# Kernel tuning notes

Hardware: AMD Instinct MI355X
Metric: run time of the kernel (lower is better)

## Reference

```python
import jax, jax.numpy as jnp
import numpy as np

SAMPLE_RATE = 24000.0
HARMONIC_NUM = 8
SINE_AMP = 0.1


def setup_inputs() -> dict:
    key = jax.random.key(0)
    k_f0, k_uv, k_w, k_b, k_n = jax.random.split(key, 5)
    batch, frames, upp = 16, 1000, 300
    f0_hz = 100.0 + 300.0 * jax.random.uniform(k_f0, (batch, frames), dtype=jnp.float32)
    voiced = jax.random.uniform(k_uv, (batch, frames)) > 0.2
    f0 = jnp.where(voiced, f0_hz, 0.0).astype(jnp.float32)
    W = jax.random.normal(k_w, (1, HARMONIC_NUM + 1), dtype=jnp.float32) / 3.0
    b = jax.random.normal(k_b, (1,), dtype=jnp.float32) * 0.01
    noise = jax.random.normal(k_n, (batch, frames * upp, 1), dtype=jnp.float32)
    return {"f0": f0, "W": W, "b": b, "noise": noise, "upp": upp}


def reference(f0, W, b, noise, upp):
    # Nearest-neighbor upsample along time: [B, F] -> [B, F*upp]
    f0_up = jnp.repeat(f0, upp, axis=1)
    # cumsum(f0 * h) == h * cumsum(f0): one scan, broadcast over harmonics.
    base_phase = jnp.cumsum(f0_up / SAMPLE_RATE, axis=1) * (2.0 * np.pi)  # [B, S]
    h = jnp.arange(1, HARMONIC_NUM + 2, dtype=f0.dtype)  # [9]
    sines = jnp.sin(base_phase[..., None] * h) * SINE_AMP  # [B, S, 9]
    uv = (f0_up > 0).astype(f0.dtype)[..., None]  # [B, S, 1]
    harmonics = sines * uv
    har_source = jnp.tanh(jnp.einsum('bsh,oh->bso', harmonics, W) + b)  # [B, S, 1]
    noise_out = noise * (SINE_AMP / 3.0)
    return har_source, noise_out, uv
```

## Files before the change

### kernel.cpp

```cpp
#include <hip/hip_runtime.h>
#include <math.h>


#define NHARM 9

typedef float f32x4 __attribute__((ext_vector_type(4)));

template <int UPP>
__global__ __launch_bounds__(256) void hnnsf_fused(
    const float* __restrict__ f0, const float* __restrict__ W,
    const float* __restrict__ bptr, const float* __restrict__ noise,
    float* __restrict__ out, int frames, int S, int N,
    double upp_over_sr, float inv_sr) {
  constexpr int SPT = 8;
  constexpr int BLK = 256;
  constexpr int CHUNK = SPT * BLK;
  const int b = blockIdx.y;
  const int t0_blk = blockIdx.x * CHUNK;
  const int tid = threadIdx.x;

  const float* f0row = f0 + b * frames;

  const int f_start = t0_blk / UPP;
  const int t_last = min(t0_blk + CHUNK - 1, S - 1);
  const int nf = t_last / UPP - f_start + 1;

  double local = 0.0;
  for (int t = tid; t < f_start; t += BLK) local += (double)f0row[t];
#pragma unroll
  for (int off = 32; off >= 1; off >>= 1) local += __shfl_down(local, off, 64);

  __shared__ double s_part[4];
  __shared__ float2 s_tab[8];
  __shared__ float s_f0[8];
  const int wid = tid >> 6, lane = tid & 63;
  if (lane == 0) s_part[wid] = local;
  if (tid < nf) s_f0[tid] = f0row[f_start + tid];
  __syncthreads();
  if (tid < nf) {
    double P = s_part[0] + s_part[1] + s_part[2] + s_part[3];
    for (int r = 0; r < tid; ++r) P += (double)s_f0[r];
    double rv = P * upp_over_sr;
    s_tab[tid] = make_float2((float)(rv - floor(rv)), s_f0[tid] * inv_sr);
  }
  __syncthreads();

  const int i0 = t0_blk + tid * SPT;
  if (i0 >= S) return;
  const int g0 = b * S + i0;

  float w[NHARM];
#pragma unroll
  for (int h = 0; h < NHARM; ++h) w[h] = W[h] * 0.1f;
  const float bias = bptr[0];
  const float nscale = (float)(0.1 / 3.0);

  const f32x4 nz0 = *reinterpret_cast<const f32x4*>(noise + g0);
  const f32x4 nz1 = *reinterpret_cast<const f32x4*>(noise + g0 + 4);

  float harr[8], uvr[8];
#pragma unroll
  for (int k = 0; k < SPT; ++k) {
    const int t = i0 + k;
    const int f = t / UPP;
    const int j = t - f * UPP;
    const float2 fr = s_tab[f - f_start];
    const float uv = (fr.y > 0.0f) ? 1.0f : 0.0f;
    const float rf = __builtin_amdgcn_fractf(fmaf(fr.y, (float)(j + 1), fr.x));

    float acc = 0.0f;
#pragma unroll
    for (int h = 1; h <= NHARM; ++h) {
      const float x = __builtin_amdgcn_fractf(rf * (float)h);
      acc = fmaf(w[h - 1], __builtin_amdgcn_sinf(x), acc);
    }
    const float z = fmaf(uv, acc, bias);
    const float z2 = z * z;
    harr[k] = z * (27.0f + z2) / fmaf(9.0f, z2, 27.0f);
    uvr[k] = uv;
  }

  *reinterpret_cast<f32x4*>(out + g0) = (f32x4){harr[0], harr[1], harr[2], harr[3]};
  *reinterpret_cast<f32x4*>(out + g0 + 4) = (f32x4){harr[4], harr[5], harr[6], harr[7]};
  *reinterpret_cast<f32x4*>(out + N + g0) = nz0 * nscale;
  *reinterpret_cast<f32x4*>(out + N + g0 + 4) = nz1 * nscale;
  *reinterpret_cast<f32x4*>(out + 2 * N + g0) = (f32x4){uvr[0], uvr[1], uvr[2], uvr[3]};
  *reinterpret_cast<f32x4*>(out + 2 * N + g0 + 4) = (f32x4){uvr[4], uvr[5], uvr[6], uvr[7]};
}

__global__ __launch_bounds__(64) void f0_scan_kernel(
    const float* __restrict__ f0, float2* __restrict__ tab, int frames,
    double upp_over_sr, float inv_sr) {
  const int b = blockIdx.x;
  const int lane = threadIdx.x;
  const int per = (frames + 63) / 64;

  double vals[16];
  double local = 0.0;
#pragma unroll
  for (int i = 0; i < 16; ++i) {
    if (i < per) {
      int f = lane * per + i;
      double v = (f < frames) ? (double)f0[b * frames + f] : 0.0;
      vals[i] = local;
      local += v;
    }
  }
  double incl = local;
#pragma unroll
  for (int off = 1; off < 64; off <<= 1) {
    double v = __shfl_up(incl, off, 64);
    if (lane >= off) incl += v;
  }
  const double excl = incl - local;
#pragma unroll
  for (int i = 0; i < 16; ++i) {
    if (i < per) {
      int f = lane * per + i;
      if (f < frames) {
        double rev = (excl + vals[i]) * upp_over_sr;
        tab[b * frames + f] =
            make_float2((float)(rev - floor(rev)), f0[b * frames + f] * inv_sr);
      }
    }
  }
}

__global__ __launch_bounds__(256) void hnnsf_generic(
    const float* __restrict__ W, const float* __restrict__ bptr,
    const float* __restrict__ noise, const float2* __restrict__ tab,
    float* __restrict__ out, int frames, int upp, int S, int N) {
  const int tid = blockIdx.x * blockDim.x + threadIdx.x;
  const int i0 = tid * 4;
  if (i0 >= N) return;
  const int b = i0 / S;
  const int t0 = i0 - b * S;

  float w[NHARM];
#pragma unroll
  for (int h = 0; h < NHARM; ++h) w[h] = W[h] * 0.1f;
  const float bias = bptr[0];
  const float nscale = (float)(0.1 / 3.0);
  const f32x4 nz = *reinterpret_cast<const f32x4*>(noise + i0);

  float harr[4], uvr[4];
#pragma unroll
  for (int k = 0; k < 4; ++k) {
    const int t = t0 + k;
    const int f = t / upp;
    const int j = t - f * upp;
    const float2 fr = tab[b * frames + f];
    const float uv = (fr.y > 0.0f) ? 1.0f : 0.0f;
    const float rf = __builtin_amdgcn_fractf(fmaf(fr.y, (float)(j + 1), fr.x));
    float acc = 0.0f;
#pragma unroll
    for (int h = 1; h <= NHARM; ++h) {
      const float x = __builtin_amdgcn_fractf(rf * (float)h);
      acc = fmaf(w[h - 1], __builtin_amdgcn_sinf(x), acc);
    }
    const float z = fmaf(uv, acc, bias);
    const float z2 = z * z;
    harr[k] = z * (27.0f + z2) / fmaf(9.0f, z2, 27.0f);
    uvr[k] = uv;
  }
  *reinterpret_cast<f32x4*>(out + i0) = (f32x4){harr[0], harr[1], harr[2], harr[3]};
  *reinterpret_cast<f32x4*>(out + N + i0) = nz * nscale;
  *reinterpret_cast<f32x4*>(out + 2 * N + i0) = (f32x4){uvr[0], uvr[1], uvr[2], uvr[3]};
}

extern "C" void kernel_launch(void* const* d_in, const int* in_sizes, int n_in,
                              void* d_out, int out_size, void* d_ws,
                              size_t ws_size, hipStream_t stream) {
  const float* f0 = (const float*)d_in[0];
  const float* W = (const float*)d_in[1];
  const float* bptr = (const float*)d_in[2];
  const float* noise = (const float*)d_in[3];
  const int BF = in_sizes[0];
  const int NS = in_sizes[3];
  const int upp = NS / BF;
  const int B = 16;
  const int frames = BF / B;
  const int S = frames * upp;
  const int N = NS;
  const double upp_over_sr = (double)upp / 24000.0;
  const float inv_sr = (float)(1.0 / 24000.0);
  float* out = (float*)d_out;

  if (upp == 300) {
    const int CHUNK = 2048;
    dim3 grid((S + CHUNK - 1) / CHUNK, B);
    hnnsf_fused<300><<<grid, 256, 0, stream>>>(f0, W, bptr, noise, out, frames,
                                               S, N, upp_over_sr, inv_sr);
  } else {
    float2* tab = (float2*)d_ws;
    f0_scan_kernel<<<B, 64, 0, stream>>>(f0, tab, frames, upp_over_sr, inv_sr);
    const int grid = (N / 4 + 255) / 256;
    hnnsf_generic<<<grid, 256, 0, stream>>>(W, bptr, noise, tab, out, frames,
                                            upp, S, N);
  }
}
```

Baseline: 21.34 us.

## Use Chebyshev harmonic recurrence, fast reciprocal, earlier noise copy, smaller chunks

The nine per-harmonic sin evaluations are replaced by one sin and one cos followed by the Chebyshev recurrence sin((h+1)x) = 2cos(x)sin(hx) - sin((h-1)x). The tanh rational approximation now uses a hardware reciprocal instead of a full-precision divide. The noise scaling copy is issued before the prefix-sum phase so its memory traffic overlaps the scan. Samples per thread drop from 8 to 4, doubling the block count to improve occupancy, at the cost of a larger per-block prefix scan over the f0 row and some recurrence rounding error.

```diff
diff --git a/kernel.cpp b/kernel.cpp
--- a/kernel.cpp
+++ b/kernel.cpp
@@ -12,7 +12,7 @@
     const float* __restrict__ bptr, const float* __restrict__ noise,
     float* __restrict__ out, int frames, int S, int N,
     double upp_over_sr, float inv_sr) {
-  constexpr int SPT = 8;
+  constexpr int SPT = 4;
   constexpr int BLK = 256;
   constexpr int CHUNK = SPT * BLK;
   const int b = blockIdx.y;
@@ -20,6 +20,15 @@
   const int tid = threadIdx.x;
 
   const float* f0row = f0 + b * frames;
+  const int i0 = t0_blk + tid * SPT;
+  const bool active = i0 < S;
+  const int g0 = b * S + i0;
+  const float nscale = (float)(0.1 / 3.0);
+
+  if (active) {
+    const f32x4 nz = *reinterpret_cast<const f32x4*>(noise + g0);
+    *reinterpret_cast<f32x4*>(out + N + g0) = nz * nscale;
+  }
 
   const int f_start = t0_blk / UPP;
   const int t_last = min(t0_blk + CHUNK - 1, S - 1);
@@ -44,21 +53,14 @@
     s_tab[tid] = make_float2((float)(rv - floor(rv)), s_f0[tid] * inv_sr);
   }
   __syncthreads();
-
-  const int i0 = t0_blk + tid * SPT;
-  if (i0 >= S) return;
-  const int g0 = b * S + i0;
+  if (!active) return;
 
   float w[NHARM];
 #pragma unroll
   for (int h = 0; h < NHARM; ++h) w[h] = W[h] * 0.1f;
   const float bias = bptr[0];
-  const float nscale = (float)(0.1 / 3.0);
-
-  const f32x4 nz0 = *reinterpret_cast<const f32x4*>(noise + g0);
-  const f32x4 nz1 = *reinterpret_cast<const f32x4*>(noise + g0 + 4);
-
-  float harr[8], uvr[8];
+
+  float harr[SPT], uvr[SPT];
 #pragma unroll
   for (int k = 0; k < SPT; ++k) {
     const int t = i0 + k;
@@ -68,24 +70,25 @@
     const float uv = (fr.y > 0.0f) ? 1.0f : 0.0f;
     const float rf = __builtin_amdgcn_fractf(fmaf(fr.y, (float)(j + 1), fr.x));
 
-    float acc = 0.0f;
-#pragma unroll
-    for (int h = 1; h <= NHARM; ++h) {
-      const float x = __builtin_amdgcn_fractf(rf * (float)h);
-      acc = fmaf(w[h - 1], __builtin_amdgcn_sinf(x), acc);
+    const float s1 = __builtin_amdgcn_sinf(rf);
+    const float c2 = 2.0f * __builtin_amdgcn_cosf(rf);
+    float sm2 = 0.0f, sm1 = s1;
+    float acc = w[0] * s1;
+#pragma unroll
+    for (int h = 2; h <= NHARM; ++h) {
+      const float sh = fmaf(c2, sm1, -sm2);
+      acc = fmaf(w[h - 1], sh, acc);
+      sm2 = sm1;
+      sm1 = sh;
     }
     const float z = fmaf(uv, acc, bias);
     const float z2 = z * z;
-    harr[k] = z * (27.0f + z2) / fmaf(9.0f, z2, 27.0f);
+    harr[k] = z * (27.0f + z2) * __builtin_amdgcn_rcpf(fmaf(9.0f, z2, 27.0f));
     uvr[k] = uv;
   }
 
   *reinterpret_cast<f32x4*>(out + g0) = (f32x4){harr[0], harr[1], harr[2], harr[3]};
-  *reinterpret_cast<f32x4*>(out + g0 + 4) = (f32x4){harr[4], harr[5], harr[6], harr[7]};
-  *reinterpret_cast<f32x4*>(out + N + g0) = nz0 * nscale;
-  *reinterpret_cast<f32x4*>(out + N + g0 + 4) = nz1 * nscale;
   *reinterpret_cast<f32x4*>(out + 2 * N + g0) = (f32x4){uvr[0], uvr[1], uvr[2], uvr[3]};
-  *reinterpret_cast<f32x4*>(out + 2 * N + g0 + 4) = (f32x4){uvr[4], uvr[5], uvr[6], uvr[7]};
 }
 
 __global__ __launch_bounds__(64) void f0_scan_kernel(
@@ -160,7 +163,7 @@
     }
     const float z = fmaf(uv, acc, bias);
     const float z2 = z * z;
-    harr[k] = z * (27.0f + z2) / fmaf(9.0f, z2, 27.0f);
+    harr[k] = z * (27.0f + z2) * __builtin_amdgcn_rcpf(fmaf(9.0f, z2, 27.0f));
     uvr[k] = uv;
   }
   *reinterpret_cast<f32x4*>(out + i0) = (f32x4){harr[0], harr[1], harr[2], harr[3]};
@@ -187,7 +190,7 @@
   float* out = (float*)d_out;
 
   if (upp == 300) {
-    const int CHUNK = 2048;
+    const int CHUNK = 1024;
     dim3 grid((S + CHUNK - 1) / CHUNK, B);
     hnnsf_fused<300><<<grid, 256, 0, stream>>>(f0, W, bptr, noise, out, frames,
                                                S, N, upp_over_sr, inv_sr);
```

New measurement: 20.69 us. -3.1%, faster.
